# Performance work log

Hardware: AMD Instinct MI355X
Metric: run time of the kernel (lower is better)

The kernel has to match this reference:

```python
import jax, jax.numpy as jnp
import numpy as np

N, E, IN_DIM, HID, L = 50000, 800000, 64, 64, 3
EDGE_DIM = 2 * HID + 2  # src_h | dst_h | edge_feat


def setup_inputs() -> dict:
    key = jax.random.key(0)
    ks = jax.random.split(key, 32)
    s = 0.05
    inp = {
        "h": jax.random.normal(ks[0], (N, IN_DIM), jnp.float32),
        "e": jax.random.normal(ks[1], (E, 2), jnp.float32),
        "src": jax.random.randint(ks[2], (E,), 0, N),
        "dst": jax.random.randint(ks[3], (E,), 0, N),
        # input embedding
        "emb_W": jax.random.normal(ks[4], (IN_DIM, HID), jnp.float32) * s,
        "emb_b": jnp.zeros((HID,), jnp.float32),
        # per-GIN-layer params (stacked over L)
        "eps": jnp.zeros((L,), jnp.float32),  # learn_eps init 0
        "mlp_W1": jax.random.normal(ks[5], (L, HID, HID), jnp.float32) * s,
        "mlp_b1": jnp.zeros((L, HID), jnp.float32),
        "mlp_bn_s": jnp.ones((L, HID), jnp.float32),   # eval-mode BN folded: x*s+sh
        "mlp_bn_sh": jnp.zeros((L, HID), jnp.float32),
        "mlp_W2": jax.random.normal(ks[6], (L, HID, HID), jnp.float32) * s,
        "mlp_b2": jnp.zeros((L, HID), jnp.float32),
        "apply_bn_s": jnp.ones((L, HID), jnp.float32),
        "apply_bn_sh": jnp.zeros((L, HID), jnp.float32),
        "gin_bn_s": jnp.ones((L, HID), jnp.float32),
        "gin_bn_sh": jnp.zeros((L, HID), jnp.float32),
        # prediction heads (L+1 of them)
        "pred_W1": jax.random.normal(ks[7], (L + 1, EDGE_DIM, HID), jnp.float32) * s,
        "pred_b1": jnp.zeros((L + 1, HID), jnp.float32),
        "pred_W2": jax.random.normal(ks[8], (L + 1, HID, 1), jnp.float32) * s,
        "pred_b2": jnp.zeros((L + 1, 1), jnp.float32),
    }
    return inp


def reference(h, e, src, dst, emb_W, emb_b, eps,
              mlp_W1, mlp_b1, mlp_bn_s, mlp_bn_sh, mlp_W2, mlp_b2,
              apply_bn_s, apply_bn_sh, gin_bn_s, gin_bn_sh,
              pred_W1, pred_b1, pred_W2, pred_b2):
    n = h.shape[0]
    bn = lambda x, sc, sh: x * sc + sh  # eval-mode batchnorm (folded scale/shift)

    h = h @ emb_W + emb_b  # [N, HID]

    def edge_feat(hh):
        # gather node features onto edges: [E, 2*HID+2]
        return jnp.concatenate([hh[src], hh[dst], e], axis=1)

    def pred(ef, i):
        z = jax.nn.relu(ef @ pred_W1[i] + pred_b1[i])
        return z @ pred_W2[i] + pred_b2[i]  # [E, 1]

    score = pred(edge_feat(h), 0)
    for i in range(L):
        h_in = h
        # GIN sum aggregation: copy src features, sum at dst
        neigh = jax.ops.segment_sum(h[src], dst, num_segments=n)
        x = (1.0 + eps[i]) * h + neigh
        # MLP: Linear -> BN -> ReLU -> Linear
        x = jax.nn.relu(bn(x @ mlp_W1[i] + mlp_b1[i], mlp_bn_s[i], mlp_bn_sh[i]))
        x = x @ mlp_W2[i] + mlp_b2[i]
        # ApplyNodeFunc: BN -> ReLU
        x = jax.nn.relu(bn(x, apply_bn_s[i], apply_bn_sh[i]))
        # GINLayer post: BN -> ReLU -> residual (dropout=0 in eval)
        x = jax.nn.relu(bn(x, gin_bn_s[i], gin_bn_sh[i]))
        h = h_in + x
        score = score + pred(edge_feat(h), i + 1)
    return jax.nn.relu(score)
```

## Files before the change

kernel.cpp:

```cpp
#include <hip/hip_runtime.h>

typedef unsigned short ushort_t;
typedef unsigned int uint_t;

static __device__ __forceinline__ ushort_t f2bf(float f) {
    uint_t u = __float_as_uint(f);
    uint_t r = (u + 0x7FFFu + ((u >> 16) & 1u)) >> 16;
    return (ushort_t)r;
}
static __device__ __forceinline__ float bf2f(ushort_t u) {
    return __uint_as_float(((uint_t)u) << 16);
}

static __device__ __forceinline__ float edge_p(
    ushort4 a, float4 brow, float ex, float ey,
    float4 wc0, float4 wc1, float4 w2v)
{
    float z0 = bf2f(a.x) + brow.x + ex*wc0.x + ey*wc1.x; z0 = fmaxf(z0, 0.f);
    float z1 = bf2f(a.y) + brow.y + ex*wc0.y + ey*wc1.y; z1 = fmaxf(z1, 0.f);
    float z2 = bf2f(a.z) + brow.z + ex*wc0.z + ey*wc1.z; z2 = fmaxf(z2, 0.f);
    float z3 = bf2f(a.w) + brow.w + ex*wc0.w + ey*wc1.w; z3 = fmaxf(z3, 0.f);
    return z0*w2v.x + z1*w2v.y + z2*w2v.z + z3*w2v.w;
}

#define RED16(p) { p += __shfl_xor(p,1); p += __shfl_xor(p,2); \
                   p += __shfl_xor(p,4); p += __shfl_xor(p,8); }

__global__ __launch_bounds__(256) void k_count(
    const int* __restrict__ dst, int* __restrict__ deg, int E)
{
    int e = blockIdx.x * 256 + threadIdx.x;
    if (e < E) atomicAdd(&deg[dst[e]], 1);
}

__global__ __launch_bounds__(1024) void k_scanA(
    const int* __restrict__ deg, int* __restrict__ partial,
    int* __restrict__ bsum, int N)
{
    __shared__ int wsum[16];
    int tid = threadIdx.x, lane = tid & 63, wid = tid >> 6;
    int idx = blockIdx.x * 1024 + tid;
    int v = (idx < N) ? deg[idx] : 0;
    int x = v;
#pragma unroll
    for (int o = 1; o < 64; o <<= 1) {
        int t = __shfl_up(x, o, 64);
        if (lane >= o) x += t;
    }
    if (lane == 63) wsum[wid] = x;
    __syncthreads();
    if (wid == 0) {
        int s = (lane < 16) ? wsum[lane] : 0;
#pragma unroll
        for (int o = 1; o < 16; o <<= 1) {
            int t = __shfl_up(s, o, 64);
            if (lane >= o) s += t;
        }
        if (lane < 16) wsum[lane] = s;
    }
    __syncthreads();
    int woff = (wid > 0) ? wsum[wid - 1] : 0;
    if (idx < N) partial[idx] = woff + x - v;
    if (tid == 0) bsum[blockIdx.x] = wsum[15];
}

__global__ __launch_bounds__(256) void k_scanB(
    int* __restrict__ bsum, int nb, int* __restrict__ totalp)
{
    __shared__ int s[256];
    int tid = threadIdx.x;
    int v = (tid < nb) ? bsum[tid] : 0;
    s[tid] = v;
    __syncthreads();
#pragma unroll
    for (int off = 1; off < 256; off <<= 1) {
        int t = (tid >= off) ? s[tid - off] : 0;
        __syncthreads();
        s[tid] += t;
        __syncthreads();
    }
    if (tid < nb) bsum[tid] = s[tid] - v;
    if (tid == 0) totalp[0] = s[255];
}

__global__ __launch_bounds__(256) void k_scanC(
    int* __restrict__ offsets, const int* __restrict__ bsum,
    int* __restrict__ cursor, int N)
{
    int idx = blockIdx.x * 256 + threadIdx.x;
    if (idx >= N) return;
    int o = offsets[idx] + bsum[idx >> 10];
    offsets[idx] = o;
    cursor[idx] = o;
}

__global__ __launch_bounds__(256) void k_fill(
    const int* __restrict__ src, const int* __restrict__ dst,
    const float* __restrict__ ep, int* __restrict__ cursor,
    int4* __restrict__ entries, int E)
{
    int ei = blockIdx.x * 256 + threadIdx.x;
    if (ei >= E) return;
    int pos = atomicAdd(&cursor[dst[ei]], 1);
    float2 ev = *(const float2*)(ep + 2 * (size_t)ei);
    entries[pos] = make_int4(src[ei], ei, __float_as_int(ev.x), __float_as_int(ev.y));
}

__global__ __launch_bounds__(256) void k_embed_ab(
    const float* __restrict__ in, const float* __restrict__ W,
    const float* __restrict__ bias, float* __restrict__ hout,
    ushort_t* __restrict__ hbfout,
    const float* __restrict__ WA, const float* __restrict__ bA,
    const float* __restrict__ WB,
    ushort_t* __restrict__ A, ushort_t* __restrict__ B, int N)
{
    __shared__ float xs[16][68];
    const int row16 = threadIdx.x >> 4;
    const int li    = threadIdx.x & 15;
    const int r     = blockIdx.x * 16 + row16;
    if (r >= N) return;
    float4 x4 = *(const float4*)(in + (size_t)r * 64 + 4 * li);
    xs[row16][4*li+0] = x4.x; xs[row16][4*li+1] = x4.y;
    xs[row16][4*li+2] = x4.z; xs[row16][4*li+3] = x4.w;
    float4 acc = *(const float4*)(bias + 4 * li);
#pragma unroll
    for (int k = 0; k < 64; k++) {
        float xk = xs[row16][k];
        float4 wv = *(const float4*)(W + k * 64 + 4 * li);
        acc.x += xk * wv.x; acc.y += xk * wv.y;
        acc.z += xk * wv.z; acc.w += xk * wv.w;
    }
    *(float4*)(hout + (size_t)r * 64 + 4 * li) = acc;
    if (hbfout) {
        ushort4 o;
        o.x = f2bf(acc.x); o.y = f2bf(acc.y); o.z = f2bf(acc.z); o.w = f2bf(acc.w);
        *(ushort4*)(hbfout + (size_t)r * 64 + 4 * li) = o;
    }
    xs[row16][4*li+0] = acc.x; xs[row16][4*li+1] = acc.y;
    xs[row16][4*li+2] = acc.z; xs[row16][4*li+3] = acc.w;
    float4 aA = *(const float4*)(bA + 4 * li);
    float4 aB = make_float4(0.f, 0.f, 0.f, 0.f);
#pragma unroll
    for (int k = 0; k < 64; k++) {
        float xk = xs[row16][k];
        float4 wa = *(const float4*)(WA + k * 64 + 4 * li);
        float4 wb = *(const float4*)(WB + k * 64 + 4 * li);
        aA.x += xk * wa.x; aA.y += xk * wa.y; aA.z += xk * wa.z; aA.w += xk * wa.w;
        aB.x += xk * wb.x; aB.y += xk * wb.y; aB.z += xk * wb.z; aB.w += xk * wb.w;
    }
    ushort4 oa, ob;
    oa.x = f2bf(aA.x); oa.y = f2bf(aA.y); oa.z = f2bf(aA.z); oa.w = f2bf(aA.w);
    ob.x = f2bf(aB.x); ob.y = f2bf(aB.y); ob.z = f2bf(aB.z); ob.w = f2bf(aB.w);
    *(ushort4*)(A + (size_t)r * 64 + 4 * li) = oa;
    *(ushort4*)(B + (size_t)r * 64 + 4 * li) = ob;
}

__global__ __launch_bounds__(256) void k_matmulAB(
    const float* __restrict__ h, const float* __restrict__ WA,
    const float* __restrict__ bA, const float* __restrict__ WB,
    ushort_t* __restrict__ A, ushort_t* __restrict__ B, int N)
{
    __shared__ float xs[16][68];
    const int row16 = threadIdx.x >> 4;
    const int li    = threadIdx.x & 15;
    const int r     = blockIdx.x * 16 + row16;
    if (r >= N) return;
    float4 x4 = *(const float4*)(h + (size_t)r * 64 + 4 * li);
    xs[row16][4*li+0] = x4.x; xs[row16][4*li+1] = x4.y;
    xs[row16][4*li+2] = x4.z; xs[row16][4*li+3] = x4.w;
    float4 accA = *(const float4*)(bA + 4 * li);
    float4 accB = make_float4(0.f, 0.f, 0.f, 0.f);
#pragma unroll
    for (int k = 0; k < 64; k++) {
        float xk = xs[row16][k];
        float4 wa = *(const float4*)(WA + k * 64 + 4 * li);
        float4 wb = *(const float4*)(WB + k * 64 + 4 * li);
        accA.x += xk * wa.x; accA.y += xk * wa.y;
        accA.z += xk * wa.z; accA.w += xk * wa.w;
        accB.x += xk * wb.x; accB.y += xk * wb.y;
        accB.z += xk * wb.z; accB.w += xk * wb.w;
    }
    ushort4 oa, ob;
    oa.x = f2bf(accA.x); oa.y = f2bf(accA.y); oa.z = f2bf(accA.z); oa.w = f2bf(accA.w);
    ob.x = f2bf(accB.x); ob.y = f2bf(accB.y); ob.z = f2bf(accB.z); ob.w = f2bf(accB.w);
    *(ushort4*)(A + (size_t)r * 64 + 4 * li) = oa;
    *(ushort4*)(B + (size_t)r * 64 + 4 * li) = ob;
}

template <int MODE, int HASGIN, int AGGBF, int EPI>
__global__ __launch_bounds__(256) void k_fused(
    const float* __restrict__ h, float* __restrict__ hout,
    const ushort_t* __restrict__ hbf, ushort_t* __restrict__ hbfout,
    const ushort_t* __restrict__ A, const ushort_t* __restrict__ Bm,
    const int4* __restrict__ entries, const int* __restrict__ offsets,
    float* __restrict__ score_csr, float* __restrict__ score_out,
    const float* __restrict__ Wc, const float* __restrict__ W2v,
    const float* __restrict__ b2p, const float* __restrict__ epsp,
    const float* __restrict__ W1, const float* __restrict__ b1,
    const float* __restrict__ s1, const float* __restrict__ sh1,
    const float* __restrict__ W2, const float* __restrict__ b2,
    const float* __restrict__ as_, const float* __restrict__ ash,
    const float* __restrict__ gs, const float* __restrict__ gsh,
    const float* __restrict__ WAn, const float* __restrict__ bAn,
    const float* __restrict__ WBn,
    ushort_t* __restrict__ Aout, ushort_t* __restrict__ Bout, int N)
{
    __shared__ float xs[16][68];
    __shared__ float ts[16][68];
    const int row16 = threadIdx.x >> 4;
    const int li    = threadIdx.x & 15;
    const int r     = blockIdx.x * 16 + row16;
    if (r >= N) return;

    const float4 wc0 = *(const float4*)(Wc + li*4);
    const float4 wc1 = *(const float4*)(Wc + 64 + li*4);
    const float4 w2v = *(const float4*)(W2v + li*4);
    const float bb2 = b2p[0];
    ushort4 bu = *(const ushort4*)(Bm + (size_t)r * 64 + li*4);
    const float4 brow = make_float4(bf2f(bu.x), bf2f(bu.y), bf2f(bu.z), bf2f(bu.w));

    const int beg = offsets[r], end = offsets[r + 1];
    float4 acc = make_float4(0.f, 0.f, 0.f, 0.f);

    int k = beg;
    for (; k + 3 < end; k += 4) {
        int4 e0 = entries[k], e1 = entries[k+1], e2 = entries[k+2], e3 = entries[k+3];
        ushort4 a0 = *(const ushort4*)(A + (size_t)e0.x * 64 + li*4);
        ushort4 a1 = *(const ushort4*)(A + (size_t)e1.x * 64 + li*4);
        ushort4 a2 = *(const ushort4*)(A + (size_t)e2.x * 64 + li*4);
        ushort4 a3 = *(const ushort4*)(A + (size_t)e3.x * 64 + li*4);
        if (HASGIN) {
            if (AGGBF) {
                ushort4 g0 = *(const ushort4*)(hbf + (size_t)e0.x * 64 + li*4);
                ushort4 g1 = *(const ushort4*)(hbf + (size_t)e1.x * 64 + li*4);
                ushort4 g2 = *(const ushort4*)(hbf + (size_t)e2.x * 64 + li*4);
                ushort4 g3 = *(const ushort4*)(hbf + (size_t)e3.x * 64 + li*4);
                acc.x += bf2f(g0.x) + bf2f(g1.x) + bf2f(g2.x) + bf2f(g3.x);
                acc.y += bf2f(g0.y) + bf2f(g1.y) + bf2f(g2.y) + bf2f(g3.y);
                acc.z += bf2f(g0.z) + bf2f(g1.z) + bf2f(g2.z) + bf2f(g3.z);
                acc.w += bf2f(g0.w) + bf2f(g1.w) + bf2f(g2.w) + bf2f(g3.w);
            } else {
                float4 g0 = *(const float4*)(h + (size_t)e0.x * 64 + li*4);
                float4 g1 = *(const float4*)(h + (size_t)e1.x * 64 + li*4);
                float4 g2 = *(const float4*)(h + (size_t)e2.x * 64 + li*4);
                float4 g3 = *(const float4*)(h + (size_t)e3.x * 64 + li*4);
                acc.x += g0.x + g1.x + g2.x + g3.x;
                acc.y += g0.y + g1.y + g2.y + g3.y;
                acc.z += g0.z + g1.z + g2.z + g3.z;
                acc.w += g0.w + g1.w + g2.w + g3.w;
            }
        }
        float p0 = edge_p(a0, brow, __int_as_float(e0.z), __int_as_float(e0.w), wc0, wc1, w2v);
        float p1 = edge_p(a1, brow, __int_as_float(e1.z), __int_as_float(e1.w), wc0, wc1, w2v);
        float p2 = edge_p(a2, brow, __int_as_float(e2.z), __int_as_float(e2.w), wc0, wc1, w2v);
        float p3 = edge_p(a3, brow, __int_as_float(e3.z), __int_as_float(e3.w), wc0, wc1, w2v);
        RED16(p0) RED16(p1) RED16(p2) RED16(p3)
        if (li == 0) {
            if (MODE == 0) {
                score_csr[k]   = p0 + bb2; score_csr[k+1] = p1 + bb2;
                score_csr[k+2] = p2 + bb2; score_csr[k+3] = p3 + bb2;
            } else if (MODE == 1) {
                score_csr[k]   += p0 + bb2; score_csr[k+1] += p1 + bb2;
                score_csr[k+2] += p2 + bb2; score_csr[k+3] += p3 + bb2;
            } else {
                score_out[e0.y] = fmaxf(score_csr[k]   + p0 + bb2, 0.f);
                score_out[e1.y] = fmaxf(score_csr[k+1] + p1 + bb2, 0.f);
                score_out[e2.y] = fmaxf(score_csr[k+2] + p2 + bb2, 0.f);
                score_out[e3.y] = fmaxf(score_csr[k+3] + p3 + bb2, 0.f);
            }
        }
    }
    for (; k < end; k++) {
        int4 e0 = entries[k];
        ushort4 a0 = *(const ushort4*)(A + (size_t)e0.x * 64 + li*4);
        if (HASGIN) {
            if (AGGBF) {
                ushort4 g0 = *(const ushort4*)(hbf + (size_t)e0.x * 64 + li*4);
                acc.x += bf2f(g0.x); acc.y += bf2f(g0.y);
                acc.z += bf2f(g0.z); acc.w += bf2f(g0.w);
            } else {
                float4 g0 = *(const float4*)(h + (size_t)e0.x * 64 + li*4);
                acc.x += g0.x; acc.y += g0.y; acc.z += g0.z; acc.w += g0.w;
            }
        }
        float p0 = edge_p(a0, brow, __int_as_float(e0.z), __int_as_float(e0.w), wc0, wc1, w2v);
        RED16(p0)
        if (li == 0) {
            if (MODE == 0)      score_csr[k] = p0 + bb2;
            else if (MODE == 1) score_csr[k] += p0 + bb2;
            else score_out[e0.y] = fmaxf(score_csr[k] + p0 + bb2, 0.f);
        }
    }

    if (!HASGIN) return;

    const float epsv = 1.0f + epsp[0];
    float4 hv = *(const float4*)(h + (size_t)r * 64 + 4 * li);
    xs[row16][4*li+0] = epsv * hv.x + acc.x;
    xs[row16][4*li+1] = epsv * hv.y + acc.y;
    xs[row16][4*li+2] = epsv * hv.z + acc.z;
    xs[row16][4*li+3] = epsv * hv.w + acc.w;

    float4 t = *(const float4*)(b1 + 4 * li);
#pragma unroll
    for (int kk = 0; kk < 64; kk++) {
        float xk = xs[row16][kk];
        float4 wv = *(const float4*)(W1 + kk * 64 + 4 * li);
        t.x += xk * wv.x; t.y += xk * wv.y; t.z += xk * wv.z; t.w += xk * wv.w;
    }
    {
        float4 sc = *(const float4*)(s1 + 4 * li);
        float4 sh = *(const float4*)(sh1 + 4 * li);
        t.x = fmaxf(t.x * sc.x + sh.x, 0.f);
        t.y = fmaxf(t.y * sc.y + sh.y, 0.f);
        t.z = fmaxf(t.z * sc.z + sh.z, 0.f);
        t.w = fmaxf(t.w * sc.w + sh.w, 0.f);
    }
    ts[row16][4*li+0] = t.x; ts[row16][4*li+1] = t.y;
    ts[row16][4*li+2] = t.z; ts[row16][4*li+3] = t.w;

    float4 u = *(const float4*)(b2 + 4 * li);
#pragma unroll
    for (int kk = 0; kk < 64; kk++) {
        float tk = ts[row16][kk];
        float4 wv = *(const float4*)(W2 + kk * 64 + 4 * li);
        u.x += tk * wv.x; u.y += tk * wv.y; u.z += tk * wv.z; u.w += tk * wv.w;
    }
    {
        float4 sc = *(const float4*)(as_ + 4 * li);
        float4 sh = *(const float4*)(ash + 4 * li);
        u.x = fmaxf(u.x * sc.x + sh.x, 0.f);
        u.y = fmaxf(u.y * sc.y + sh.y, 0.f);
        u.z = fmaxf(u.z * sc.z + sh.z, 0.f);
        u.w = fmaxf(u.w * sc.w + sh.w, 0.f);
        sc = *(const float4*)(gs + 4 * li);
        sh = *(const float4*)(gsh + 4 * li);
        u.x = fmaxf(u.x * sc.x + sh.x, 0.f);
        u.y = fmaxf(u.y * sc.y + sh.y, 0.f);
        u.z = fmaxf(u.z * sc.z + sh.z, 0.f);
        u.w = fmaxf(u.w * sc.w + sh.w, 0.f);
    }
    float4 o = make_float4(hv.x + u.x, hv.y + u.y, hv.z + u.z, hv.w + u.w);
    *(float4*)(hout + (size_t)r * 64 + 4 * li) = o;
    if (AGGBF) {
        ushort4 ob;
        ob.x = f2bf(o.x); ob.y = f2bf(o.y); ob.z = f2bf(o.z); ob.w = f2bf(o.w);
        *(ushort4*)(hbfout + (size_t)r * 64 + 4 * li) = ob;
    }

    if (EPI) {
        xs[row16][4*li+0] = o.x; xs[row16][4*li+1] = o.y;
        xs[row16][4*li+2] = o.z; xs[row16][4*li+3] = o.w;
        float4 aA = *(const float4*)(bAn + 4 * li);
        float4 aB = make_float4(0.f, 0.f, 0.f, 0.f);
#pragma unroll
        for (int kk = 0; kk < 64; kk++) {
            float xk = xs[row16][kk];
            float4 wa = *(const float4*)(WAn + kk * 64 + 4 * li);
            float4 wb = *(const float4*)(WBn + kk * 64 + 4 * li);
            aA.x += xk * wa.x; aA.y += xk * wa.y; aA.z += xk * wa.z; aA.w += xk * wa.w;
            aB.x += xk * wb.x; aB.y += xk * wb.y; aB.z += xk * wb.z; aB.w += xk * wb.w;
        }
        ushort4 oa, ob;
        oa.x = f2bf(aA.x); oa.y = f2bf(aA.y); oa.z = f2bf(aA.z); oa.w = f2bf(aA.w);
        ob.x = f2bf(aB.x); ob.y = f2bf(aB.y); ob.z = f2bf(aB.z); ob.w = f2bf(aB.w);
        *(ushort4*)(Aout + (size_t)r * 64 + li*4) = oa;
        *(ushort4*)(Bout + (size_t)r * 64 + li*4) = ob;
    }
}

extern "C" void kernel_launch(void* const* d_in, const int* in_sizes, int n_in,
                              void* d_out, int out_size, void* d_ws, size_t ws_size,
                              hipStream_t stream) {
    const float* h_in  = (const float*)d_in[0];
    const float* e     = (const float*)d_in[1];
    const int*   src   = (const int*)d_in[2];
    const int*   dst   = (const int*)d_in[3];
    const float* emb_W = (const float*)d_in[4];
    const float* emb_b = (const float*)d_in[5];
    const float* eps   = (const float*)d_in[6];
    const float* mW1   = (const float*)d_in[7];
    const float* mb1   = (const float*)d_in[8];
    const float* mbs   = (const float*)d_in[9];
    const float* mbsh  = (const float*)d_in[10];
    const float* mW2   = (const float*)d_in[11];
    const float* mb2   = (const float*)d_in[12];
    const float* as_   = (const float*)d_in[13];
    const float* ash   = (const float*)d_in[14];
    const float* gs    = (const float*)d_in[15];
    const float* gsh   = (const float*)d_in[16];
    const float* pW1   = (const float*)d_in[17];
    const float* pb1   = (const float*)d_in[18];
    const float* pW2   = (const float*)d_in[19];
    const float* pb2   = (const float*)d_in[20];

    const int N  = in_sizes[0] / 64;
    const int E  = in_sizes[2];
    const int Lr = in_sizes[6];
    const size_t nrow = (size_t)N * 64;

    float* score = (float*)d_out;

    char* wp = (char*)d_ws;
    auto take = [&](size_t b) -> char* {
        char* p = wp; wp += (b + 255) & ~(size_t)255; return p;
    };
    float*    h0        = (float*)take(nrow * 4);
    float*    h1        = (float*)take(nrow * 4);
    ushort_t* A0        = (ushort_t*)take(nrow * 2);
    ushort_t* B0        = (ushort_t*)take(nrow * 2);
    int4*     entries   = (int4*)take((size_t)E * 16);
    float*    score_csr = (float*)take((size_t)E * 4);
    int*      offsets   = (int*)take((size_t)(N + 1) * 4);
    int*      cursor    = (int*)take((size_t)N * 4);
    int*      bsum      = (int*)take(1024);
    ushort_t* hbf0      = (ushort_t*)take(nrow * 2);
    ushort_t* hbf1      = (ushort_t*)take(nrow * 2);
    size_t need_bf = (size_t)(wp - (char*)d_ws);
    ushort_t* A1        = (ushort_t*)take(nrow * 2);
    ushort_t* B1        = (ushort_t*)take(nrow * 2);
    size_t need_epi = (size_t)(wp - (char*)d_ws);

    const bool use_bf  = ws_size >= need_bf;
    const bool use_epi = ws_size >= need_epi;
    if (!use_bf) { hbf0 = nullptr; hbf1 = nullptr; }

    const int rowBlocks = (N + 15) / 16;
    const int edgeGrid  = (E + 255) / 256;
    const int nb        = (N + 1023) / 1024;

    hipMemsetAsync(cursor, 0, (size_t)N * sizeof(int), stream);
    k_count<<<edgeGrid, 256, 0, stream>>>(dst, cursor, E);
    k_scanA<<<nb, 1024, 0, stream>>>(cursor, offsets, bsum, N);
    k_scanB<<<1, 256, 0, stream>>>(bsum, nb, offsets + N);
    k_scanC<<<(N + 255) / 256, 256, 0, stream>>>(offsets, bsum, cursor, N);
    k_fill<<<edgeGrid, 256, 0, stream>>>(src, dst, e, cursor, entries, E);

    k_embed_ab<<<rowBlocks, 256, 0, stream>>>(
        h_in, emb_W, emb_b, h0, hbf0, pW1, pb1, pW1 + 64 * 64, A0, B0, N);

    float* hcur = h0;      float* hnext = h1;
    ushort_t* bcur = hbf0; ushort_t* bnext = hbf1;
    ushort_t* Acur = A0;   ushort_t* Bcur = B0;
    ushort_t* Aalt = use_epi ? A1 : A0;
    ushort_t* Balt = use_epi ? B1 : B0;

    for (int i = 0; i < Lr; i++) {
        const float* pw  = pW1 + (size_t)i * 130 * 64;
        const float* Wc  = pw + 128 * 64;
        const float* w2  = pW2 + (size_t)i * 64;
        const float* b2  = pb2 + i;
        const float* pwn = pW1 + (size_t)(i + 1) * 130 * 64;
        const float* gW1 = mW1 + (size_t)i * 64 * 64;
        const float* gW2 = mW2 + (size_t)i * 64 * 64;

        if (use_epi) {
            if (i == 0)
                k_fused<0,1,1,1><<<rowBlocks, 256, 0, stream>>>(
                    hcur, hnext, bcur, bnext, Acur, Bcur, entries, offsets,
                    score_csr, nullptr, Wc, w2, b2, eps + i,
                    gW1, mb1 + i*64, mbs + i*64, mbsh + i*64, gW2, mb2 + i*64,
                    as_ + i*64, ash + i*64, gs + i*64, gsh + i*64,
                    pwn, pb1 + (i+1)*64, pwn + 64*64, Aalt, Balt, N);
            else
                k_fused<1,1,1,1><<<rowBlocks, 256, 0, stream>>>(
                    hcur, hnext, bcur, bnext, Acur, Bcur, entries, offsets,
                    score_csr, nullptr, Wc, w2, b2, eps + i,
                    gW1, mb1 + i*64, mbs + i*64, mbsh + i*64, gW2, mb2 + i*64,
                    as_ + i*64, ash + i*64, gs + i*64, gsh + i*64,
                    pwn, pb1 + (i+1)*64, pwn + 64*64, Aalt, Balt, N);
            { ushort_t* t = Acur; Acur = Aalt; Aalt = t; }
            { ushort_t* t = Bcur; Bcur = Balt; Balt = t; }
        } else if (use_bf) {
            if (i == 0)
                k_fused<0,1,1,0><<<rowBlocks, 256, 0, stream>>>(
                    hcur, hnext, bcur, bnext, Acur, Bcur, entries, offsets,
                    score_csr, nullptr, Wc, w2, b2, eps + i,
                    gW1, mb1 + i*64, mbs + i*64, mbsh + i*64, gW2, mb2 + i*64,
                    as_ + i*64, ash + i*64, gs + i*64, gsh + i*64,
                    nullptr, nullptr, nullptr, nullptr, nullptr, N);
            else
                k_fused<1,1,1,0><<<rowBlocks, 256, 0, stream>>>(
                    hcur, hnext, bcur, bnext, Acur, Bcur, entries, offsets,
                    score_csr, nullptr, Wc, w2, b2, eps + i,
                    gW1, mb1 + i*64, mbs + i*64, mbsh + i*64, gW2, mb2 + i*64,
                    as_ + i*64, ash + i*64, gs + i*64, gsh + i*64,
                    nullptr, nullptr, nullptr, nullptr, nullptr, N);
            k_matmulAB<<<rowBlocks, 256, 0, stream>>>(
                hnext, pwn, pb1 + (i+1)*64, pwn + 64*64, A0, B0, N);
        } else {
            if (i == 0)
                k_fused<0,1,0,0><<<rowBlocks, 256, 0, stream>>>(
                    hcur, hnext, bcur, bnext, Acur, Bcur, entries, offsets,
                    score_csr, nullptr, Wc, w2, b2, eps + i,
                    gW1, mb1 + i*64, mbs + i*64, mbsh + i*64, gW2, mb2 + i*64,
                    as_ + i*64, ash + i*64, gs + i*64, gsh + i*64,
                    nullptr, nullptr, nullptr, nullptr, nullptr, N);
            else
                k_fused<1,1,0,0><<<rowBlocks, 256, 0, stream>>>(
                    hcur, hnext, bcur, bnext, Acur, Bcur, entries, offsets,
                    score_csr, nullptr, Wc, w2, b2, eps + i,
                    gW1, mb1 + i*64, mbs + i*64, mbsh + i*64, gW2, mb2 + i*64,
                    as_ + i*64, ash + i*64, gs + i*64, gsh + i*64,
                    nullptr, nullptr, nullptr, nullptr, nullptr, N);
            k_matmulAB<<<rowBlocks, 256, 0, stream>>>(
                hnext, pwn, pb1 + (i+1)*64, pwn + 64*64, A0, B0, N);
        }
        { float* t = hcur; hcur = hnext; hnext = t; }
        { ushort_t* t = bcur; bcur = bnext; bnext = t; }
    }

    {
        const float* pw = pW1 + (size_t)Lr * 130 * 64;
        const float* Wc = pw + 128 * 64;
        const float* w2 = pW2 + (size_t)Lr * 64;
        const float* b2 = pb2 + Lr;
        k_fused<2,0,0,0><<<rowBlocks, 256, 0, stream>>>(
            hcur, nullptr, nullptr, nullptr, Acur, Bcur, entries, offsets,
            score_csr, score, Wc, w2, b2, nullptr,
            nullptr, nullptr, nullptr, nullptr, nullptr, nullptr,
            nullptr, nullptr, nullptr, nullptr,
            nullptr, nullptr, nullptr, nullptr, nullptr, N);
    }
}
```

Measured before the change: 616.4 us.

## Interleave A and bf16 h into one gather table, process 4 edges per wave

Merges the per-node A projection and bf16 copy of h into one 128-element interleaved row so each edge gather is a single 16-byte load covering both. Each wave now owns one destination row and loads 64 CSR entries cooperatively, broadcasting them with shuffles so the four 16-lane slots handle different edges in parallel. Partial neighbour sums are reduced across slots before the MLP, which now runs one output column per lane. The goal is fewer, wider gathers and more edge-level parallelism per node, at the cost of extra shuffles and less work per wave on low-degree rows.

Result: slower. 854.0 us (+38.5%).

```diff
diff --git a/kernel.cpp b/kernel.cpp
--- a/kernel.cpp
+++ b/kernel.cpp
@@ -11,16 +11,14 @@
 static __device__ __forceinline__ float bf2f(ushort_t u) {
     return __uint_as_float(((uint_t)u) << 16);
 }
-
-static __device__ __forceinline__ float edge_p(
-    ushort4 a, float4 brow, float ex, float ey,
-    float4 wc0, float4 wc1, float4 w2v)
-{
-    float z0 = bf2f(a.x) + brow.x + ex*wc0.x + ey*wc1.x; z0 = fmaxf(z0, 0.f);
-    float z1 = bf2f(a.y) + brow.y + ex*wc0.y + ey*wc1.y; z1 = fmaxf(z1, 0.f);
-    float z2 = bf2f(a.z) + brow.z + ex*wc0.z + ey*wc1.z; z2 = fmaxf(z2, 0.f);
-    float z3 = bf2f(a.w) + brow.w + ex*wc0.w + ey*wc1.w; z3 = fmaxf(z3, 0.f);
-    return z0*w2v.x + z1*w2v.y + z2*w2v.z + z3*w2v.w;
+static __device__ __forceinline__ float bf2f_lo(uint_t u) {
+    return __uint_as_float(u << 16);
+}
+static __device__ __forceinline__ float bf2f_hi(uint_t u) {
+    return __uint_as_float(u & 0xffff0000u);
+}
+static __device__ __forceinline__ uint_t pack2(float lo, float hi) {
+    return (uint_t)f2bf(lo) | ((uint_t)f2bf(hi) << 16);
 }
 
 #define RED16(p) { p += __shfl_xor(p,1); p += __shfl_xor(p,2); \
@@ -106,92 +104,79 @@
     entries[pos] = make_int4(src[ei], ei, __float_as_int(ev.x), __float_as_int(ev.y));
 }
 
+static __device__ __forceinline__ void epi_tables(
+    float (*xs)[64], int wv, int lane, int li, int slot, int r, float o,
+    const float* __restrict__ WAn, const float* __restrict__ bAn,
+    const float* __restrict__ WBn,
+    ushort_t* __restrict__ comb_out, ushort_t* __restrict__ B_out)
+{
+    xs[wv][lane] = o;
+    float an = bAn[lane];
+    float bn = 0.f;
+#pragma unroll
+    for (int k = 0; k < 64; k++) {
+        float ok = xs[wv][k];
+        an += ok * WAn[k * 64 + lane];
+        bn += ok * WBn[k * 64 + lane];
+    }
+    B_out[(size_t)r * 64 + lane] = f2bf(bn);
+    float a0 = __shfl(an, 4*li+0), a1 = __shfl(an, 4*li+1);
+    float a2 = __shfl(an, 4*li+2), a3 = __shfl(an, 4*li+3);
+    float g0 = __shfl(o,  4*li+0), g1 = __shfl(o,  4*li+1);
+    float g2 = __shfl(o,  4*li+2), g3 = __shfl(o,  4*li+3);
+    if (slot == 0) {
+        int4 cw;
+        cw.x = (int)pack2(a0, a1);
+        cw.y = (int)pack2(a2, a3);
+        cw.z = (int)pack2(g0, g1);
+        cw.w = (int)pack2(g2, g3);
+        *(int4*)(comb_out + (size_t)r * 128 + li * 8) = cw;
+    }
+}
+
 __global__ __launch_bounds__(256) void k_embed_ab(
     const float* __restrict__ in, const float* __restrict__ W,
     const float* __restrict__ bias, float* __restrict__ hout,
-    ushort_t* __restrict__ hbfout,
     const float* __restrict__ WA, const float* __restrict__ bA,
     const float* __restrict__ WB,
-    ushort_t* __restrict__ A, ushort_t* __restrict__ B, int N)
-{
-    __shared__ float xs[16][68];
-    const int row16 = threadIdx.x >> 4;
-    const int li    = threadIdx.x & 15;
-    const int r     = blockIdx.x * 16 + row16;
+    ushort_t* __restrict__ comb_out, ushort_t* __restrict__ B_out, int N)
+{
+    __shared__ float xs[4][64];
+    const int wv   = threadIdx.x >> 6;
+    const int lane = threadIdx.x & 63;
+    const int li   = lane & 15;
+    const int slot = lane >> 4;
+    const int r    = blockIdx.x * 4 + wv;
     if (r >= N) return;
-    float4 x4 = *(const float4*)(in + (size_t)r * 64 + 4 * li);
-    xs[row16][4*li+0] = x4.x; xs[row16][4*li+1] = x4.y;
-    xs[row16][4*li+2] = x4.z; xs[row16][4*li+3] = x4.w;
-    float4 acc = *(const float4*)(bias + 4 * li);
-#pragma unroll
-    for (int k = 0; k < 64; k++) {
-        float xk = xs[row16][k];
-        float4 wv = *(const float4*)(W + k * 64 + 4 * li);
-        acc.x += xk * wv.x; acc.y += xk * wv.y;
-        acc.z += xk * wv.z; acc.w += xk * wv.w;
-    }
-    *(float4*)(hout + (size_t)r * 64 + 4 * li) = acc;
-    if (hbfout) {
-        ushort4 o;
-        o.x = f2bf(acc.x); o.y = f2bf(acc.y); o.z = f2bf(acc.z); o.w = f2bf(acc.w);
-        *(ushort4*)(hbfout + (size_t)r * 64 + 4 * li) = o;
-    }
-    xs[row16][4*li+0] = acc.x; xs[row16][4*li+1] = acc.y;
-    xs[row16][4*li+2] = acc.z; xs[row16][4*li+3] = acc.w;
-    float4 aA = *(const float4*)(bA + 4 * li);
-    float4 aB = make_float4(0.f, 0.f, 0.f, 0.f);
-#pragma unroll
-    for (int k = 0; k < 64; k++) {
-        float xk = xs[row16][k];
-        float4 wa = *(const float4*)(WA + k * 64 + 4 * li);
-        float4 wb = *(const float4*)(WB + k * 64 + 4 * li);
-        aA.x += xk * wa.x; aA.y += xk * wa.y; aA.z += xk * wa.z; aA.w += xk * wa.w;
-        aB.x += xk * wb.x; aB.y += xk * wb.y; aB.z += xk * wb.z; aB.w += xk * wb.w;
-    }
-    ushort4 oa, ob;
-    oa.x = f2bf(aA.x); oa.y = f2bf(aA.y); oa.z = f2bf(aA.z); oa.w = f2bf(aA.w);
-    ob.x = f2bf(aB.x); ob.y = f2bf(aB.y); ob.z = f2bf(aB.z); ob.w = f2bf(aB.w);
-    *(ushort4*)(A + (size_t)r * 64 + 4 * li) = oa;
-    *(ushort4*)(B + (size_t)r * 64 + 4 * li) = ob;
-}
-
-__global__ __launch_bounds__(256) void k_matmulAB(
-    const float* __restrict__ h, const float* __restrict__ WA,
-    const float* __restrict__ bA, const float* __restrict__ WB,
-    ushort_t* __restrict__ A, ushort_t* __restrict__ B, int N)
-{
-    __shared__ float xs[16][68];
-    const int row16 = threadIdx.x >> 4;
-    const int li    = threadIdx.x & 15;
-    const int r     = blockIdx.x * 16 + row16;
+    xs[wv][lane] = in[(size_t)r * 64 + lane];
+    float acc = bias[lane];
+#pragma unroll
+    for (int k = 0; k < 64; k++) acc += xs[wv][k] * W[k * 64 + lane];
+    hout[(size_t)r * 64 + lane] = acc;
+    epi_tables(xs, wv, lane, li, slot, r, acc, WA, bA, WB, comb_out, B_out);
+}
+
+__global__ __launch_bounds__(256) void k_tables(
+    const float* __restrict__ h,
+    const float* __restrict__ WA, const float* __restrict__ bA,
+    const float* __restrict__ WB,
+    ushort_t* __restrict__ comb_out, ushort_t* __restrict__ B_out, int N)
+{
+    __shared__ float xs[4][64];
+    const int wv   = threadIdx.x >> 6;
+    const int lane = threadIdx.x & 63;
+    const int li   = lane & 15;
+    const int slot = lane >> 4;
+    const int r    = blockIdx.x * 4 + wv;
     if (r >= N) return;
-    float4 x4 = *(const float4*)(h + (size_t)r * 64 + 4 * li);
-    xs[row16][4*li+0] = x4.x; xs[row16][4*li+1] = x4.y;
-    xs[row16][4*li+2] = x4.z; xs[row16][4*li+3] = x4.w;
-    float4 accA = *(const float4*)(bA + 4 * li);
-    float4 accB = make_float4(0.f, 0.f, 0.f, 0.f);
-#pragma unroll
-    for (int k = 0; k < 64; k++) {
-        float xk = xs[row16][k];
-        float4 wa = *(const float4*)(WA + k * 64 + 4 * li);
-        float4 wb = *(const float4*)(WB + k * 64 + 4 * li);
-        accA.x += xk * wa.x; accA.y += xk * wa.y;
-        accA.z += xk * wa.z; accA.w += xk * wa.w;
-        accB.x += xk * wb.x; accB.y += xk * wb.y;
-        accB.z += xk * wb.z; accB.w += xk * wb.w;
-    }
-    ushort4 oa, ob;
-    oa.x = f2bf(accA.x); oa.y = f2bf(accA.y); oa.z = f2bf(accA.z); oa.w = f2bf(accA.w);
-    ob.x = f2bf(accB.x); ob.y = f2bf(accB.y); ob.z = f2bf(accB.z); ob.w = f2bf(accB.w);
-    *(ushort4*)(A + (size_t)r * 64 + 4 * li) = oa;
-    *(ushort4*)(B + (size_t)r * 64 + 4 * li) = ob;
-}
-
-template <int MODE, int HASGIN, int AGGBF, int EPI>
+    float o = h[(size_t)r * 64 + lane];
+    epi_tables(xs, wv, lane, li, slot, r, o, WA, bA, WB, comb_out, B_out);
+}
+
+template <int MODE, int HASGIN, int EPI>
 __global__ __launch_bounds__(256) void k_fused(
     const float* __restrict__ h, float* __restrict__ hout,
-    const ushort_t* __restrict__ hbf, ushort_t* __restrict__ hbfout,
-    const ushort_t* __restrict__ A, const ushort_t* __restrict__ Bm,
+    const ushort_t* __restrict__ comb, const ushort_t* __restrict__ Bm,
     const int4* __restrict__ entries, const int* __restrict__ offsets,
     float* __restrict__ score_csr, float* __restrict__ score_out,
     const float* __restrict__ Wc, const float* __restrict__ W2v,
@@ -203,13 +188,14 @@
     const float* __restrict__ gs, const float* __restrict__ gsh,
     const float* __restrict__ WAn, const float* __restrict__ bAn,
     const float* __restrict__ WBn,
-    ushort_t* __restrict__ Aout, ushort_t* __restrict__ Bout, int N)
-{
-    __shared__ float xs[16][68];
-    __shared__ float ts[16][68];
-    const int row16 = threadIdx.x >> 4;
-    const int li    = threadIdx.x & 15;
-    const int r     = blockIdx.x * 16 + row16;
+    ushort_t* __restrict__ comb_out, ushort_t* __restrict__ B_out, int N)
+{
+    __shared__ float xs[4][64];
+    const int wv   = threadIdx.x >> 6;
+    const int lane = threadIdx.x & 63;
+    const int li   = lane & 15;
+    const int slot = lane >> 4;
+    const int r    = blockIdx.x * 4 + wv;
     if (r >= N) return;
 
     const float4 wc0 = *(const float4*)(Wc + li*4);
@@ -220,153 +206,118 @@
     const float4 brow = make_float4(bf2f(bu.x), bf2f(bu.y), bf2f(bu.z), bf2f(bu.w));
 
     const int beg = offsets[r], end = offsets[r + 1];
+    const int deg = end - beg;
     float4 acc = make_float4(0.f, 0.f, 0.f, 0.f);
 
-    int k = beg;
-    for (; k + 3 < end; k += 4) {
-        int4 e0 = entries[k], e1 = entries[k+1], e2 = entries[k+2], e3 = entries[k+3];
-        ushort4 a0 = *(const ushort4*)(A + (size_t)e0.x * 64 + li*4);
-        ushort4 a1 = *(const ushort4*)(A + (size_t)e1.x * 64 + li*4);
-        ushort4 a2 = *(const ushort4*)(A + (size_t)e2.x * 64 + li*4);
-        ushort4 a3 = *(const ushort4*)(A + (size_t)e3.x * 64 + li*4);
-        if (HASGIN) {
-            if (AGGBF) {
-                ushort4 g0 = *(const ushort4*)(hbf + (size_t)e0.x * 64 + li*4);
-                ushort4 g1 = *(const ushort4*)(hbf + (size_t)e1.x * 64 + li*4);
-                ushort4 g2 = *(const ushort4*)(hbf + (size_t)e2.x * 64 + li*4);
-                ushort4 g3 = *(const ushort4*)(hbf + (size_t)e3.x * 64 + li*4);
-                acc.x += bf2f(g0.x) + bf2f(g1.x) + bf2f(g2.x) + bf2f(g3.x);
-                acc.y += bf2f(g0.y) + bf2f(g1.y) + bf2f(g2.y) + bf2f(g3.y);
-                acc.z += bf2f(g0.z) + bf2f(g1.z) + bf2f(g2.z) + bf2f(g3.z);
-                acc.w += bf2f(g0.w) + bf2f(g1.w) + bf2f(g2.w) + bf2f(g3.w);
-            } else {
-                float4 g0 = *(const float4*)(h + (size_t)e0.x * 64 + li*4);
-                float4 g1 = *(const float4*)(h + (size_t)e1.x * 64 + li*4);
-                float4 g2 = *(const float4*)(h + (size_t)e2.x * 64 + li*4);
-                float4 g3 = *(const float4*)(h + (size_t)e3.x * 64 + li*4);
-                acc.x += g0.x + g1.x + g2.x + g3.x;
-                acc.y += g0.y + g1.y + g2.y + g3.y;
-                acc.z += g0.z + g1.z + g2.z + g3.z;
-                acc.w += g0.w + g1.w + g2.w + g3.w;
+    for (int base = 0; base < deg; base += 64) {
+        const int nb = min(64, deg - base);
+        int4 ent = make_int4(0, 0, 0, 0);
+        if (lane < nb) ent = entries[beg + base + lane];
+
+        int j0 = 0;
+        for (; j0 + 8 <= nb; j0 += 8) {
+            const int ja = j0 + slot;
+            const int jb = j0 + 4 + slot;
+            int   sa = __shfl(ent.x, ja);
+            int   sb = __shfl(ent.x, jb);
+            int   ea = __shfl(ent.y, ja);
+            int   eb = __shfl(ent.y, jb);
+            float xa = __int_as_float(__shfl(ent.z, ja));
+            float xb = __int_as_float(__shfl(ent.z, jb));
+            float ya = __int_as_float(__shfl(ent.w, ja));
+            float yb = __int_as_float(__shfl(ent.w, jb));
+            int4 ca = *(const int4*)(comb + (size_t)sa * 128 + li * 8);
+            int4 cb = *(const int4*)(comb + (size_t)sb * 128 + li * 8);
+            if (HASGIN) {
+                acc.x += bf2f_lo(ca.z) + bf2f_lo(cb.z);
+                acc.y += bf2f_hi(ca.z) + bf2f_hi(cb.z);
+                acc.z += bf2f_lo(ca.w) + bf2f_lo(cb.w);
+                acc.w += bf2f_hi(ca.w) + bf2f_hi(cb.w);
+            }
+            float z0 = bf2f_lo(ca.x) + brow.x + xa*wc0.x + ya*wc1.x; z0 = fmaxf(z0, 0.f);
+            float z1 = bf2f_hi(ca.x) + brow.y + xa*wc0.y + ya*wc1.y; z1 = fmaxf(z1, 0.f);
+            float z2 = bf2f_lo(ca.y) + brow.z + xa*wc0.z + ya*wc1.z; z2 = fmaxf(z2, 0.f);
+            float z3 = bf2f_hi(ca.y) + brow.w + xa*wc0.w + ya*wc1.w; z3 = fmaxf(z3, 0.f);
+            float pa = z0*w2v.x + z1*w2v.y + z2*w2v.z + z3*w2v.w;
+            z0 = bf2f_lo(cb.x) + brow.x + xb*wc0.x + yb*wc1.x; z0 = fmaxf(z0, 0.f);
+            z1 = bf2f_hi(cb.x) + brow.y + xb*wc0.y + yb*wc1.y; z1 = fmaxf(z1, 0.f);
+            z2 = bf2f_lo(cb.y) + brow.z + xb*wc0.z + yb*wc1.z; z2 = fmaxf(z2, 0.f);
+            z3 = bf2f_hi(cb.y) + brow.w + xb*wc0.w + yb*wc1.w; z3 = fmaxf(z3, 0.f);
+            float pb = z0*w2v.x + z1*w2v.y + z2*w2v.z + z3*w2v.w;
+            RED16(pa) RED16(pb)
+            if (li == 0) {
+                int ka = beg + base + ja;
+                int kb = beg + base + jb;
+                if (MODE == 0) {
+                    score_csr[ka] = pa + bb2;
+                    score_csr[kb] = pb + bb2;
+                } else if (MODE == 1) {
+                    score_csr[ka] += pa + bb2;
+                    score_csr[kb] += pb + bb2;
+                } else {
+                    score_out[ea] = fmaxf(score_csr[ka] + pa + bb2, 0.f);
+                    score_out[eb] = fmaxf(score_csr[kb] + pb + bb2, 0.f);
+                }
             }
         }
-        float p0 = edge_p(a0, brow, __int_as_float(e0.z), __int_as_float(e0.w), wc0, wc1, w2v);
-        float p1 = edge_p(a1, brow, __int_as_float(e1.z), __int_as_float(e1.w), wc0, wc1, w2v);
-        float p2 = edge_p(a2, brow, __int_as_float(e2.z), __int_as_float(e2.w), wc0, wc1, w2v);
-        float p3 = edge_p(a3, brow, __int_as_float(e3.z), __int_as_float(e3.w), wc0, wc1, w2v);
-        RED16(p0) RED16(p1) RED16(p2) RED16(p3)
-        if (li == 0) {
-            if (MODE == 0) {
-                score_csr[k]   = p0 + bb2; score_csr[k+1] = p1 + bb2;
-                score_csr[k+2] = p2 + bb2; score_csr[k+3] = p3 + bb2;
-            } else if (MODE == 1) {
-                score_csr[k]   += p0 + bb2; score_csr[k+1] += p1 + bb2;
-                score_csr[k+2] += p2 + bb2; score_csr[k+3] += p3 + bb2;
-            } else {
-                score_out[e0.y] = fmaxf(score_csr[k]   + p0 + bb2, 0.f);
-                score_out[e1.y] = fmaxf(score_csr[k+1] + p1 + bb2, 0.f);
-                score_out[e2.y] = fmaxf(score_csr[k+2] + p2 + bb2, 0.f);
-                score_out[e3.y] = fmaxf(score_csr[k+3] + p3 + bb2, 0.f);
+        for (; j0 < nb; j0 += 4) {
+            const int j  = j0 + slot;
+            const bool ok = (j < nb);
+            const int jc = ok ? j : (nb - 1);
+            int   sa = __shfl(ent.x, jc);
+            int   ea = __shfl(ent.y, jc);
+            float xa = __int_as_float(__shfl(ent.z, jc));
+            float ya = __int_as_float(__shfl(ent.w, jc));
+            int4 ca = *(const int4*)(comb + (size_t)sa * 128 + li * 8);
+            if (HASGIN && ok) {
+                acc.x += bf2f_lo(ca.z); acc.y += bf2f_hi(ca.z);
+                acc.z += bf2f_lo(ca.w); acc.w += bf2f_hi(ca.w);
+            }
+            float z0 = bf2f_lo(ca.x) + brow.x + xa*wc0.x + ya*wc1.x; z0 = fmaxf(z0, 0.f);
+            float z1 = bf2f_hi(ca.x) + brow.y + xa*wc0.y + ya*wc1.y; z1 = fmaxf(z1, 0.f);
+            float z2 = bf2f_lo(ca.y) + brow.z + xa*wc0.z + ya*wc1.z; z2 = fmaxf(z2, 0.f);
+            float z3 = bf2f_hi(ca.y) + brow.w + xa*wc0.w + ya*wc1.w; z3 = fmaxf(z3, 0.f);
+            float p = z0*w2v.x + z1*w2v.y + z2*w2v.z + z3*w2v.w;
+            RED16(p)
+            if (li == 0 && ok) {
+                int ka = beg + base + j;
+                if (MODE == 0)      score_csr[ka] = p + bb2;
+                else if (MODE == 1) score_csr[ka] += p + bb2;
+                else score_out[ea] = fmaxf(score_csr[ka] + p + bb2, 0.f);
             }
         }
     }
-    for (; k < end; k++) {
-        int4 e0 = entries[k];
-        ushort4 a0 = *(const ushort4*)(A + (size_t)e0.x * 64 + li*4);
-        if (HASGIN) {
-            if (AGGBF) {
-                ushort4 g0 = *(const ushort4*)(hbf + (size_t)e0.x * 64 + li*4);
-                acc.x += bf2f(g0.x); acc.y += bf2f(g0.y);
-                acc.z += bf2f(g0.z); acc.w += bf2f(g0.w);
-            } else {
-                float4 g0 = *(const float4*)(h + (size_t)e0.x * 64 + li*4);
-                acc.x += g0.x; acc.y += g0.y; acc.z += g0.z; acc.w += g0.w;
-            }
-        }
-        float p0 = edge_p(a0, brow, __int_as_float(e0.z), __int_as_float(e0.w), wc0, wc1, w2v);
-        RED16(p0)
-        if (li == 0) {
-            if (MODE == 0)      score_csr[k] = p0 + bb2;
-            else if (MODE == 1) score_csr[k] += p0 + bb2;
-            else score_out[e0.y] = fmaxf(score_csr[k] + p0 + bb2, 0.f);
-        }
-    }
 
     if (!HASGIN) return;
 
+    acc.x += __shfl_xor(acc.x, 16); acc.x += __shfl_xor(acc.x, 32);
+    acc.y += __shfl_xor(acc.y, 16); acc.y += __shfl_xor(acc.y, 32);
+    acc.z += __shfl_xor(acc.z, 16); acc.z += __shfl_xor(acc.z, 32);
+    acc.w += __shfl_xor(acc.w, 16); acc.w += __shfl_xor(acc.w, 32);
+    if (slot == 0) *(float4*)(&xs[wv][li * 4]) = acc;
+
     const float epsv = 1.0f + epsp[0];
-    float4 hv = *(const float4*)(h + (size_t)r * 64 + 4 * li);
-    xs[row16][4*li+0] = epsv * hv.x + acc.x;
-    xs[row16][4*li+1] = epsv * hv.y + acc.y;
-    xs[row16][4*li+2] = epsv * hv.z + acc.z;
-    xs[row16][4*li+3] = epsv * hv.w + acc.w;
-
-    float4 t = *(const float4*)(b1 + 4 * li);
-#pragma unroll
-    for (int kk = 0; kk < 64; kk++) {
-        float xk = xs[row16][kk];
-        float4 wv = *(const float4*)(W1 + kk * 64 + 4 * li);
-        t.x += xk * wv.x; t.y += xk * wv.y; t.z += xk * wv.z; t.w += xk * wv.w;
-    }
-    {
-        float4 sc = *(const float4*)(s1 + 4 * li);
-        float4 sh = *(const float4*)(sh1 + 4 * li);
-        t.x = fmaxf(t.x * sc.x + sh.x, 0.f);
-        t.y = fmaxf(t.y * sc.y + sh.y, 0.f);
-        t.z = fmaxf(t.z * sc.z + sh.z, 0.f);
-        t.w = fmaxf(t.w * sc.w + sh.w, 0.f);
-    }
-    ts[row16][4*li+0] = t.x; ts[row16][4*li+1] = t.y;
-    ts[row16][4*li+2] = t.z; ts[row16][4*li+3] = t.w;
-
-    float4 u = *(const float4*)(b2 + 4 * li);
-#pragma unroll
-    for (int kk = 0; kk < 64; kk++) {
-        float tk = ts[row16][kk];
-        float4 wv = *(const float4*)(W2 + kk * 64 + 4 * li);
-        u.x += tk * wv.x; u.y += tk * wv.y; u.z += tk * wv.z; u.w += tk * wv.w;
-    }
-    {
-        float4 sc = *(const float4*)(as_ + 4 * li);
-        float4 sh = *(const float4*)(ash + 4 * li);
-        u.x = fmaxf(u.x * sc.x + sh.x, 0.f);
-        u.y = fmaxf(u.y * sc.y + sh.y, 0.f);
-        u.z = fmaxf(u.z * sc.z + sh.z, 0.f);
-        u.w = fmaxf(u.w * sc.w + sh.w, 0.f);
-        sc = *(const float4*)(gs + 4 * li);
-        sh = *(const float4*)(gsh + 4 * li);
-        u.x = fmaxf(u.x * sc.x + sh.x, 0.f);
-        u.y = fmaxf(u.y * sc.y + sh.y, 0.f);
-        u.z = fmaxf(u.z * sc.z + sh.z, 0.f);
-        u.w = fmaxf(u.w * sc.w + sh.w, 0.f);
-    }
-    float4 o = make_float4(hv.x + u.x, hv.y + u.y, hv.z + u.z, hv.w + u.w);
-    *(float4*)(hout + (size_t)r * 64 + 4 * li) = o;
-    if (AGGBF) {
-        ushort4 ob;
-        ob.x = f2bf(o.x); ob.y = f2bf(o.y); ob.z = f2bf(o.z); ob.w = f2bf(o.w);
-        *(ushort4*)(hbfout + (size_t)r * 64 + 4 * li) = ob;
-    }
-
-    if (EPI) {
-        xs[row16][4*li+0] = o.x; xs[row16][4*li+1] = o.y;
-        xs[row16][4*li+2] = o.z; xs[row16][4*li+3] = o.w;
-        float4 aA = *(const float4*)(bAn + 4 * li);
-        float4 aB = make_float4(0.f, 0.f, 0.f, 0.f);
-#pragma unroll
-        for (int kk = 0; kk < 64; kk++) {
-            float xk = xs[row16][kk];
-            float4 wa = *(const float4*)(WAn + kk * 64 + 4 * li);
-            float4 wb = *(const float4*)(WBn + kk * 64 + 4 * li);
-            aA.x += xk * wa.x; aA.y += xk * wa.y; aA.z += xk * wa.z; aA.w += xk * wa.w;
-            aB.x += xk * wb.x; aB.y += xk * wb.y; aB.z += xk * wb.z; aB.w += xk * wb.w;
-        }
-        ushort4 oa, ob;
-        oa.x = f2bf(aA.x); oa.y = f2bf(aA.y); oa.z = f2bf(aA.z); oa.w = f2bf(aA.w);
-        ob.x = f2bf(aB.x); ob.y = f2bf(aB.y); ob.z = f2bf(aB.z); ob.w = f2bf(aB.w);
-        *(ushort4*)(Aout + (size_t)r * 64 + li*4) = oa;
-        *(ushort4*)(Bout + (size_t)r * 64 + li*4) = ob;
-    }
+    const float hself = h[(size_t)r * 64 + lane];
+    float x = epsv * hself + xs[wv][lane];
+    xs[wv][lane] = x;
+
+    float t = b1[lane];
+#pragma unroll
+    for (int k = 0; k < 64; k++) t += xs[wv][k] * W1[k * 64 + lane];
+    t = fmaxf(t * s1[lane] + sh1[lane], 0.f);
+    xs[wv][lane] = t;
+
+    float u = b2[lane];
+#pragma unroll
+    for (int k = 0; k < 64; k++) u += xs[wv][k] * W2[k * 64 + lane];
+    u = fmaxf(u * as_[lane] + ash[lane], 0.f);
+    u = fmaxf(u * gs[lane] + gsh[lane], 0.f);
+
+    float o = hself + u;
+    hout[(size_t)r * 64 + lane] = o;
+
+    if (EPI)
+        epi_tables(xs, wv, lane, li, slot, r, o, WAn, bAn, WBn, comb_out, B_out);
 }
 
 extern "C" void kernel_launch(void* const* d_in, const int* in_sizes, int n_in,
@@ -407,27 +358,24 @@
     };
     float*    h0        = (float*)take(nrow * 4);
     float*    h1        = (float*)take(nrow * 4);
-    ushort_t* A0        = (ushort_t*)take(nrow * 2);
+    ushort_t* comb0     = (ushort_t*)take(nrow * 4);
     ushort_t* B0        = (ushort_t*)take(nrow * 2);
     int4*     entries   = (int4*)take((size_t)E * 16);
     float*    score_csr = (float*)take((size_t)E * 4);
     int*      offsets   = (int*)take((size_t)(N + 1) * 4);
     int*      cursor    = (int*)take((size_t)N * 4);
     int*      bsum      = (int*)take(1024);
-    ushort_t* hbf0      = (ushort_t*)take(nrow * 2);
-    ushort_t* hbf1      = (ushort_t*)take(nrow * 2);
-    size_t need_bf = (size_t)(wp - (char*)d_ws);
-    ushort_t* A1        = (ushort_t*)take(nrow * 2);
+    size_t need_base = (size_t)(wp - (char*)d_ws);
+    ushort_t* comb1     = (ushort_t*)take(nrow * 4);
     ushort_t* B1        = (ushort_t*)take(nrow * 2);
     size_t need_epi = (size_t)(wp - (char*)d_ws);
-
-    const bool use_bf  = ws_size >= need_bf;
+    (void)need_base;
+
     const bool use_epi = ws_size >= need_epi;
-    if (!use_bf) { hbf0 = nullptr; hbf1 = nullptr; }
-
-    const int rowBlocks = (N + 15) / 16;
-    const int edgeGrid  = (E + 255) / 256;
-    const int nb        = (N + 1023) / 1024;
+
+    const int fusedBlocks = (N + 3) / 4;
+    const int edgeGrid    = (E + 255) / 256;
+    const int nb          = (N + 1023) / 1024;
 
     hipMemsetAsync(cursor, 0, (size_t)N * sizeof(int), stream);
     k_count<<<edgeGrid, 256, 0, stream>>>(dst, cursor, E);
@@ -436,14 +384,12 @@
     k_scanC<<<(N + 255) / 256, 256, 0, stream>>>(offsets, bsum, cursor, N);
     k_fill<<<edgeGrid, 256, 0, stream>>>(src, dst, e, cursor, entries, E);
 
-    k_embed_ab<<<rowBlocks, 256, 0, stream>>>(
-        h_in, emb_W, emb_b, h0, hbf0, pW1, pb1, pW1 + 64 * 64, A0, B0, N);
-
-    float* hcur = h0;      float* hnext = h1;
-    ushort_t* bcur = hbf0; ushort_t* bnext = hbf1;
-    ushort_t* Acur = A0;   ushort_t* Bcur = B0;
-    ushort_t* Aalt = use_epi ? A1 : A0;
-    ushort_t* Balt = use_epi ? B1 : B0;
+    k_embed_ab<<<fusedBlocks, 256, 0, stream>>>(
+        h_in, emb_W, emb_b, h0, pW1, pb1, pW1 + 64 * 64, comb0, B0, N);
+
+    float* hcur = h0;       float* hnext = h1;
+    ushort_t* Ccur = comb0; ushort_t* Cnxt = use_epi ? comb1 : comb0;
+    ushort_t* Bcur = B0;    ushort_t* Bnxt = use_epi ? B1 : B0;
 
     for (int i = 0; i < Lr; i++) {
         const float* pw  = pW1 + (size_t)i * 130 * 64;
@@ -456,58 +402,40 @@
 
         if (use_epi) {
             if (i == 0)
-                k_fused<0,1,1,1><<<rowBlocks, 256, 0, stream>>>(
-                    hcur, hnext, bcur, bnext, Acur, Bcur, entries, offsets,
-                    score_csr, nullptr, Wc, w2, b2, eps + i,
+                k_fused<0,1,1><<<fusedBlocks, 256, 0, stream>>>(
+                    hcur, hnext, Ccur, Bcur, entries, offsets, score_csr, nullptr,
+                    Wc, w2, b2, eps + i,
                     gW1, mb1 + i*64, mbs + i*64, mbsh + i*64, gW2, mb2 + i*64,
                     as_ + i*64, ash + i*64, gs + i*64, gsh + i*64,
-                    pwn, pb1 + (i+1)*64, pwn + 64*64, Aalt, Balt, N);
+                    pwn, pb1 + (i+1)*64, pwn + 64*64, Cnxt, Bnxt, N);
             else
-                k_fused<1,1,1,1><<<rowBlocks, 256, 0, stream>>>(
-                    hcur, hnext, bcur, bnext, Acur, Bcur, entries, offsets,
-                    score_csr, nullptr, Wc, w2, b2, eps + i,
+                k_fused<1,1,1><<<fusedBlocks, 256, 0, stream>>>(
+                    hcur, hnext, Ccur, Bcur, entries, offsets, score_csr, nullptr,
+                    Wc, w2, b2, eps + i,
                     gW1, mb1 + i*64, mbs + i*64, mbsh + i*64, gW2, mb2 + i*64,
                     as_ + i*64, ash + i*64, gs + i*64, gsh + i*64,
-                    pwn, pb1 + (i+1)*64, pwn + 64*64, Aalt, Balt, N);
-            { ushort_t* t = Acur; Acur = Aalt; Aalt = t; }
-            { ushort_t* t = Bcur; Bcur = Balt; Balt = t; }
-        } else if (use_bf) {
+                    pwn, pb1 + (i+1)*64, pwn + 64*64, Cnxt, Bnxt, N);
+            { ushort_t* t = Ccur; Ccur = Cnxt; Cnxt = t; }
+            { ushort_t* t = Bcur; Bcur = Bnxt; Bnxt = t; }
+        } else {
             if (i == 0)
-                k_fused<0,1,1,0><<<rowBlocks, 256, 0, stream>>>(
-                    hcur, hnext, bcur, bnext, Acur, Bcur, entries, offsets,
-                    score_csr, nullptr, Wc, w2, b2, eps + i,
+                k_fused<0,1,0><<<fusedBlocks, 256, 0, stream>>>(
+                    hcur, hnext, Ccur, Bcur, entries, offsets, score_csr, nullptr,
+                    Wc, w2, b2, eps + i,
                     gW1, mb1 + i*64, mbs + i*64, mbsh + i*64, gW2, mb2 + i*64,
                     as_ + i*64, ash + i*64, gs + i*64, gsh + i*64,
                     nullptr, nullptr, nullptr, nullptr, nullptr, N);
             else
-                k_fused<1,1,1,0><<<rowBlocks, 256, 0, stream>>>(
-                    hcur, hnext, bcur, bnext, Acur, Bcur, entries, offsets,
-                    score_csr, nullptr, Wc, w2, b2, eps + i,
+                k_fused<1,1,0><<<fusedBlocks, 256, 0, stream>>>(
+                    hcur, hnext, Ccur, Bcur, entries, offsets, score_csr, nullptr,
+                    Wc, w2, b2, eps + i,
                     gW1, mb1 + i*64, mbs + i*64, mbsh + i*64, gW2, mb2 + i*64,
                     as_ + i*64, ash + i*64, gs + i*64, gsh + i*64,
                     nullptr, nullptr, nullptr, nullptr, nullptr, N);
-            k_matmulAB<<<rowBlocks, 256, 0, stream>>>(
-                hnext, pwn, pb1 + (i+1)*64, pwn + 64*64, A0, B0, N);
-        } else {
-            if (i == 0)
-                k_fused<0,1,0,0><<<rowBlocks, 256, 0, stream>>>(
-                    hcur, hnext, bcur, bnext, Acur, Bcur, entries, offsets,
-                    score_csr, nullptr, Wc, w2, b2, eps + i,
-                    gW1, mb1 + i*64, mbs + i*64, mbsh + i*64, gW2, mb2 + i*64,
-                    as_ + i*64, ash + i*64, gs + i*64, gsh + i*64,
-                    nullptr, nullptr, nullptr, nullptr, nullptr, N);
-            else
-                k_fused<1,1,0,0><<<rowBlocks, 256, 0, stream>>>(
-                    hcur, hnext, bcur, bnext, Acur, Bcur, entries, offsets,
-                    score_csr, nullptr, Wc, w2, b2, eps + i,
-                    gW1, mb1 + i*64, mbs + i*64, mbsh + i*64, gW2, mb2 + i*64,
-                    as_ + i*64, ash + i*64, gs + i*64, gsh + i*64,
-                    nullptr, nullptr, nullptr, nullptr, nullptr, N);
-            k_matmulAB<<<rowBlocks, 256, 0, stream>>>(
-                hnext, pwn, pb1 + (i+1)*64, pwn + 64*64, A0, B0, N);
+            k_tables<<<fusedBlocks, 256, 0, stream>>>(
+                hnext, pwn, pb1 + (i+1)*64, pwn + 64*64, Ccur, Bcur, N);
         }
         { float* t = hcur; hcur = hnext; hnext = t; }
-        { ushort_t* t = bcur; bcur = bnext; bnext = t; }
     }
 
     {
@@ -515,9 +443,9 @@
         const float* Wc = pw + 128 * 64;
         const float* w2 = pW2 + (size_t)Lr * 64;
         const float* b2 = pb2 + Lr;
-        k_fused<2,0,0,0><<<rowBlocks, 256, 0, stream>>>(
-            hcur, nullptr, nullptr, nullptr, Acur, Bcur, entries, offsets,
-            score_csr, score, Wc, w2, b2, nullptr,
+        k_fused<2,0,0><<<fusedBlocks, 256, 0, stream>>>(
+            hcur, nullptr, Ccur, Bcur, entries, offsets, score_csr, score,
+            Wc, w2, b2, nullptr,
             nullptr, nullptr, nullptr, nullptr, nullptr, nullptr,
             nullptr, nullptr, nullptr, nullptr,
             nullptr, nullptr, nullptr, nullptr, nullptr, N);
```
